# Kernel tuning notes

Measured on AMD Instinct MI355X. Metric: run time of the kernel, lower is better.

Reference implementation:

```python
import jax, jax.numpy as jnp
import numpy as np
import math

B, L, LC = 2, 2048, 2048
D_MODEL, D_CROSS, D_HEAD = 1024, 1024, 64
N_HEADS = D_MODEL // D_HEAD
D6 = D_HEAD // 6  # freq bands per spatial axis (k-diffusion AxialRoPE, 3 axes)
EPS = 1e-6


def rope_freqs():
    n = N_HEADS * D6
    f = jnp.exp(jnp.linspace(math.log(math.pi), math.log(10.0 * math.pi), n + 1)[:-1])
    return f.reshape(D6, N_HEADS).T  # [nh, d6]


def rope_theta(pos):
    # pos: [b, l, 3] -> theta: [b, nh, l, 3*d6]
    f = rope_freqs()
    th = jnp.concatenate([pos[..., None, a:a + 1] * f for a in range(3)], axis=-1)  # [b,l,nh,3*d6]
    return jnp.moveaxis(th, -2, -3)


def apply_rotary(x, theta):
    d = theta.shape[-1]
    x1, x2, x3 = x[..., :d], x[..., d:2 * d], x[..., 2 * d:]
    c, s = jnp.cos(theta), jnp.sin(theta)
    return jnp.concatenate([x1 * c - x2 * s, x2 * c + x1 * s, x3], axis=-1)


def rms_norm(x, scale, eps=EPS):
    ms = jnp.mean(x * x, axis=-1, keepdims=True)
    return x * (scale * jax.lax.rsqrt(ms + eps))


def cosine_scale(q, k, scale, eps=EPS):
    s = jnp.sqrt(scale)[:, None, None]  # [nh,1,1]
    qn = q * (s * jax.lax.rsqrt(jnp.sum(q * q, axis=-1, keepdims=True) + eps))
    kn = k * (s * jax.lax.rsqrt(jnp.sum(k * k, axis=-1, keepdims=True) + eps))
    return qn, kn


def setup_inputs():
    key = jax.random.key(0)
    ks = jax.random.split(key, 8)
    return {
        "x": jax.random.normal(ks[0], (B, L, D_MODEL), jnp.float32),
        "pos": jax.random.uniform(ks[1], (B, L, 3), jnp.float32),
        "x_cross": jax.random.normal(ks[2], (B, LC, D_CROSS), jnp.float32),
        "pos_cross": jax.random.uniform(ks[3], (B, LC, 3), jnp.float32),
        "norm_scale": jnp.ones((D_MODEL,), jnp.float32),
        "norm_cross_scale": jnp.ones((D_CROSS,), jnp.float32),
        "q_w": jax.random.normal(ks[4], (D_MODEL, D_MODEL), jnp.float32) * 0.02,
        "kv_w": jax.random.normal(ks[5], (2 * D_MODEL, D_CROSS), jnp.float32) * 0.02,
        "head_scale": jnp.full((N_HEADS,), 10.0, jnp.float32),
        "out_w": jax.random.normal(ks[6], (D_MODEL, D_MODEL), jnp.float32) * 0.02,
    }


def reference(x, pos, x_cross, pos_cross, norm_scale, norm_cross_scale, q_w, kv_w, head_scale, out_w):
    skip = x
    xn = rms_norm(x, norm_scale)
    xc = rms_norm(x_cross, norm_cross_scale)
    q = xn @ q_w.T                       # [b,l,d]
    kv = xc @ kv_w.T                     # [b,lc,2d]
    b, l, _ = q.shape
    lc = kv.shape[1]
    q = q.reshape(b, l, N_HEADS, D_HEAD).transpose(0, 2, 1, 3)          # [b,nh,l,e]
    kv = kv.reshape(b, lc, 2, N_HEADS, D_HEAD)                          # (t nh e) factorization
    k = kv[:, :, 0].transpose(0, 2, 1, 3)
    v = kv[:, :, 1].transpose(0, 2, 1, 3)
    q, k = cosine_scale(q, k, head_scale)
    q = apply_rotary(q, rope_theta(pos))
    k = apply_rotary(k, rope_theta(pos_cross))
    attn = jax.nn.softmax(jnp.einsum('bhqe,bhke->bhqk', q, k), axis=-1)  # scale=1.0 (cosine-sim pre-scaled)
    o = jnp.einsum('bhqk,bhke->bhqe', attn, v)
    o = o.transpose(0, 2, 1, 3).reshape(b, l, D_MODEL)
    return o @ out_w.T + skip
```

## Files before the change

kernel.cpp:

```cpp
#include <hip/hip_runtime.h>

typedef __bf16 bf16_t;
typedef __bf16 bf16x4 __attribute__((ext_vector_type(4)));
typedef __bf16 bf16x8 __attribute__((ext_vector_type(8)));
typedef float f32x4 __attribute__((ext_vector_type(4)));
typedef short s16x4 __attribute__((ext_vector_type(4)));

#define B_DIM 2
#define L_DIM 2048
#define LC_DIM 2048
#define DM 1024
#define NH 16
#define DH 64
#define MB (1u << 20)
#define LOG2E 1.44269504088896f
#define NZ 2
#define SPAN (LC_DIM / NZ)

__device__ __forceinline__ bool probe_is_f32(const unsigned* probe) {
  return probe[0] == 0x3F800000u;
}

__device__ __forceinline__ void async16(const bf16_t* g, bf16_t* l) {
  __builtin_amdgcn_global_load_lds((const __attribute__((address_space(1))) void*)g,
                                   (__attribute__((address_space(3))) void*)l, 16, 0, 0);
}

__device__ __forceinline__ f32x4 mfma16(bf16x4 a, bf16x4 b, f32x4 c) {
#if __has_builtin(__builtin_amdgcn_mfma_f32_16x16x16bf16_1k)
  union { bf16x4 h; s16x4 s; } ua, ub;
  ua.h = a; ub.h = b;
  return __builtin_amdgcn_mfma_f32_16x16x16bf16_1k(ua.s, ub.s, c, 0, 0, 0);
#else
  return c;
#endif
}

__device__ __forceinline__ void conv_b(const void* src, bf16_t* dst, int i, bool f32) {
  bf16x4 w;
  if (f32) {
    f32x4 v = *(const f32x4*)((const float*)src + i);
    w[0] = (bf16_t)v[0]; w[1] = (bf16_t)v[1]; w[2] = (bf16_t)v[2]; w[3] = (bf16_t)v[3];
  } else {
    w = *(const bf16x4*)((const bf16_t*)src + i);
  }
  *(bf16x4*)(dst + i) = w;
}
__device__ __forceinline__ void conv_f(const void* src, float* dst, int i, int n, bool f32) {
  if (i >= n) return;
  f32x4 v;
  if (f32) {
    v = *(const f32x4*)((const float*)src + i);
  } else {
    bf16x4 w = *(const bf16x4*)((const bf16_t*)src + i);
    v[0] = (float)w[0]; v[1] = (float)w[1]; v[2] = (float)w[2]; v[3] = (float)w[3];
  }
  *(f32x4*)(dst + i) = v;
}

__global__ __launch_bounds__(256) void front_k(
    const void* x, const void* xc, const void* qw, const void* kvw, const void* ow,
    const void* pos, const void* posc, const void* ns, const void* ncs, const void* hs,
    bf16_t* xn, bf16_t* xcn, bf16_t* cqw, bf16_t* ckvw, bf16_t* cow,
    float* fpos, float* fposc, float* fns, float* fncs, float* fhs,
    const unsigned* probe) {
  const bool f32 = probe_is_f32(probe);
  const int tid = threadIdx.x;
  if (blockIdx.x < 2 * B_DIM * L_DIM) {
    const bool isB = blockIdx.x >= B_DIM * L_DIM;
    const int row = isB ? blockIdx.x - B_DIM * L_DIM : blockIdx.x;
    const void* src = isB ? xc : x;
    const void* scr = isB ? ncs : ns;
    bf16_t* out = isB ? xcn : xn;
    float f0, f1, f2, f3, s0, s1, s2, s3;
    if (f32) {
      f32x4 v = *((const f32x4*)((const float*)src + (size_t)row * DM) + tid);
      f0 = v[0]; f1 = v[1]; f2 = v[2]; f3 = v[3];
      f32x4 sv = *((const f32x4*)scr + tid);
      s0 = sv[0]; s1 = sv[1]; s2 = sv[2]; s3 = sv[3];
    } else {
      bf16x4 v = *((const bf16x4*)((const bf16_t*)src + (size_t)row * DM) + tid);
      f0 = (float)v[0]; f1 = (float)v[1]; f2 = (float)v[2]; f3 = (float)v[3];
      bf16x4 sv = *((const bf16x4*)scr + tid);
      s0 = (float)sv[0]; s1 = (float)sv[1]; s2 = (float)sv[2]; s3 = (float)sv[3];
    }
    float ss = f0 * f0 + f1 * f1 + f2 * f2 + f3 * f3;
#pragma unroll
    for (int m = 1; m < 64; m <<= 1) ss += __shfl_xor(ss, m, 64);
    __shared__ float red[4];
    const int wave = tid >> 6, lane = tid & 63;
    if (lane == 0) red[wave] = ss;
    __syncthreads();
    float ms = (red[0] + red[1] + red[2] + red[3]) * (1.0f / DM);
    float r = rsqrtf(ms + 1e-6f);
    bf16x4 w;
    w[0] = (bf16_t)(f0 * r * s0);
    w[1] = (bf16_t)(f1 * r * s1);
    w[2] = (bf16_t)(f2 * r * s2);
    w[3] = (bf16_t)(f3 * r * s3);
    *(bf16x4*)(out + (size_t)row * DM + tid * 4) = w;
    return;
  }
  const int blk = blockIdx.x - 2 * B_DIM * L_DIM;
  const int e4 = tid * 4;
  if (blk < 1024)       conv_b(qw,  cqw,  blk * 1024 + e4, f32);
  else if (blk < 3072)  conv_b(kvw, ckvw, (blk - 1024) * 1024 + e4, f32);
  else if (blk < 4096)  conv_b(ow,  cow,  (blk - 3072) * 1024 + e4, f32);
  else if (blk < 4108)  conv_f(pos,  fpos,  (blk - 4096) * 1024 + e4, 12288, f32);
  else if (blk < 4120)  conv_f(posc, fposc, (blk - 4108) * 1024 + e4, 12288, f32);
  else if (blk == 4120) conv_f(ns,  fns,  e4, 1024, f32);
  else if (blk == 4121) conv_f(ncs, fncs, e4, 1024, f32);
  else                  conv_f(hs,  fhs,  e4, 16, f32);
}

__global__ __launch_bounds__(256) void gemm_qkv_k(const bf16_t* __restrict__ xn,
                                                  const bf16_t* __restrict__ xcn,
                                                  const bf16_t* __restrict__ qw,
                                                  const bf16_t* __restrict__ kvw,
                                                  bf16_t* __restrict__ qb,
                                                  bf16_t* __restrict__ kvK,
                                                  bf16_t* __restrict__ Vp) {
  __shared__ bf16_t Asm[128 * 32];
  __shared__ bf16_t Wsm[128 * 32];
  const int tid = threadIdx.x;
  const int wave = tid >> 6, lane = tid & 63;
  const int quad = lane >> 4, tc = lane & 15;
  const int wr = wave >> 1, wc = wave & 1;
  const bool isq = blockIdx.y < 8;
  const bf16_t* A = isq ? xn : xcn;
  const bf16_t* W = isq ? qw : kvw;
  const int n0 = (isq ? blockIdx.y : (blockIdx.y - 8)) * 128;
  const int m0 = blockIdx.x * 128;
  const int K = 1024;

  const int srow = wave * 16 + (lane >> 2);
  const int scol = (lane & 3) * 8;
  const bf16_t* ag = A + (size_t)(m0 + srow) * K + scol;
  const bf16_t* wg = W + (size_t)(n0 + srow) * K + scol;
  bf16_t* al0 = &Asm[(wave * 16) * 32];
  bf16_t* al1 = &Asm[(64 + wave * 16) * 32];
  bf16_t* wl0 = &Wsm[(wave * 16) * 32];
  bf16_t* wl1 = &Wsm[(64 + wave * 16) * 32];

  f32x4 acc[4][4] = {};

  for (int k0 = 0; k0 < K; k0 += 32) {
    async16(ag + k0, al0);
    async16(ag + k0 + (size_t)64 * K, al1);
    async16(wg + k0, wl0);
    async16(wg + k0 + (size_t)64 * K, wl1);
    __syncthreads();
    bf16x8 af[4], wf[4];
#pragma unroll
    for (int i = 0; i < 4; ++i)
      af[i] = *(const bf16x8*)&Asm[(wr * 64 + i * 16 + tc) * 32 + quad * 8];
#pragma unroll
    for (int j = 0; j < 4; ++j)
      wf[j] = *(const bf16x8*)&Wsm[(wc * 64 + j * 16 + tc) * 32 + quad * 8];
#pragma unroll
    for (int i = 0; i < 4; ++i)
#pragma unroll
      for (int j = 0; j < 4; ++j)
        acc[i][j] = __builtin_amdgcn_mfma_f32_16x16x32_bf16(af[i], wf[j], acc[i][j], 0, 0, 0);
    __syncthreads();
  }

  if (isq || n0 < DM) {
    bf16_t* C = isq ? qb : kvK;
#pragma unroll
    for (int i = 0; i < 4; ++i) {
      const size_t row = (size_t)m0 + wr * 64 + i * 16 + quad * 4;
#pragma unroll
      for (int j = 0; j < 4; ++j) {
        const int col = n0 + wc * 64 + j * 16 + tc;
#pragma unroll
        for (int r = 0; r < 4; ++r)
          C[(row + r) * DM + col] = (bf16_t)acc[i][j][r];
      }
    }
  } else {
#pragma unroll
    for (int i = 0; i < 4; ++i) {
      const int row = m0 + wr * 64 + i * 16 + quad * 4;
      const int b = row >> 11, kc = row & (LC_DIM - 1);
#pragma unroll
      for (int j = 0; j < 4; ++j) {
        const int hd = n0 - DM + wc * 64 + j * 16 + tc;
        const int h = hd >> 6, d = hd & 63;
        bf16x4 pk;
        pk[0] = (bf16_t)acc[i][j][0];
        pk[1] = (bf16_t)acc[i][j][1];
        pk[2] = (bf16_t)acc[i][j][2];
        pk[3] = (bf16_t)acc[i][j][3];
        *(bf16x4*)(Vp + (((size_t)(b * NH + h) * (LC_DIM / 4) + (kc >> 2)) * DH + d) * 4) = pk;
      }
    }
  }
}

__global__ __launch_bounds__(256) void prep_k(bf16_t* __restrict__ q,
                                              const bf16_t* __restrict__ kvK,
                                              bf16_t* __restrict__ Kp,
                                              const float* __restrict__ pos,
                                              const float* __restrict__ pos_cross,
                                              const float* __restrict__ head_scale) {
  const int gw = (blockIdx.x * blockDim.x + threadIdx.x) >> 6;
  const int lane = threadIdx.x & 63;
  const int per = B_DIM * L_DIM * NH;
  const bool is_k = gw >= per;
  const int id = is_k ? gw - per : gw;
  const int h = id & 15;
  const int row = id >> 4;
  const bf16_t* src = (is_k ? kvK : q) + (size_t)row * DM + h * DH;
  const float* pp = (is_k ? pos_cross : pos) + (size_t)row * 3;

  float val = (float)src[lane];
  float ss = val * val;
#pragma unroll
  for (int m = 1; m < 64; m <<= 1) ss += __shfl_xor(ss, m, 64);
  float sc = sqrtf(head_scale[h]) * rsqrtf(ss + 1e-6f);
  if (!is_k) sc *= LOG2E;
  float vn = val * sc;

  const int j = lane;
  const int tj = j < 30 ? j : (j < 60 ? j - 30 : 0);
  const int a = tj >= 20 ? 2 : (tj >= 10 ? 1 : 0);
  const int jj = tj - a * 10;
  float p = pp[a];
  float freq = 3.14159265358979f *
               __builtin_amdgcn_exp2f((float)(jj * 16 + h) * 0.0207620505930f);
  float rev = p * freq * 0.15915494309189535f;
  rev -= floorf(rev);
  float cth = __builtin_amdgcn_cosf(rev);
  float sth = __builtin_amdgcn_sinf(rev);
  const int partner = j < 30 ? j + 30 : (j < 60 ? j - 30 : j);
  float vp = __shfl(vn, partner, 64);
  float outv;
  if (j < 30)       outv = vn * cth - vp * sth;
  else if (j < 60)  outv = vn * cth + vp * sth;
  else              outv = vn;

  if (is_k) {
    const int b = row >> 11, l = row & (LC_DIM - 1);
    const int dsw = (((lane >> 3) ^ (l & 7)) << 3) | (lane & 7);
    Kp[(((size_t)b * NH + h) * LC_DIM + l) * DH + dsw] = (bf16_t)outv;
  } else {
    q[(size_t)row * DM + h * DH + lane] = (bf16_t)outv;
  }
}

#define STAGE14(BUF, KC)                                                         \
  {                                                                              \
    const bf16_t* ks_ = kg + (size_t)(KC) * DH;                                  \
    const bf16_t* vs_ = vg + (size_t)((KC) >> 2) * (DH * 4);                     \
    const int so_ = wave * 1024 + lane * 8;                                      \
    async16(ks_ + so_, &Kl[BUF][wave * 1024]);                                   \
    async16(ks_ + so_ + 512, &Kl[BUF][wave * 1024 + 512]);                       \
    async16(vs_ + so_, &Vl[BUF][wave * 1024]);                                   \
    async16(vs_ + so_ + 512, &Vl[BUF][wave * 1024 + 512]);                       \
  }

#define COMPUTE14(BUF)                                                           \
  {                                                                              \
    bf16x8 KB[4][2];                                                             \
    _Pragma("unroll") for (int mt = 0; mt < 4; ++mt)                             \
      _Pragma("unroll") for (int hf = 0; hf < 2; ++hf)                           \
        KB[mt][hf] = *(const bf16x8*)&Kl[BUF][(mt * 16 + tc) * 64 +              \
                                              (((hf << 2) | quad) ^ (tc & 7)) * 8]; \
    bf16x4 p[2][4];                                                              \
    _Pragma("unroll") for (int qg = 0; qg < 2; ++qg) {                           \
      f32x4 s[4];                                                                \
      _Pragma("unroll") for (int mt = 0; mt < 4; ++mt) {                         \
        f32x4 zf = {0.f, 0.f, 0.f, 0.f};                                         \
        zf = __builtin_amdgcn_mfma_f32_16x16x32_bf16(KB[mt][0], qf[qg][0], zf, 0, 0, 0); \
        zf = __builtin_amdgcn_mfma_f32_16x16x32_bf16(KB[mt][1], qf[qg][1], zf, 0, 0, 0); \
        s[mt] = zf;                                                              \
      }                                                                          \
      _Pragma("unroll") for (int mt = 0; mt < 4; ++mt) {                         \
        p[qg][mt][0] = (bf16_t)__builtin_amdgcn_exp2f(s[mt][0]);                 \
        p[qg][mt][1] = (bf16_t)__builtin_amdgcn_exp2f(s[mt][1]);                 \
        p[qg][mt][2] = (bf16_t)__builtin_amdgcn_exp2f(s[mt][2]);                 \
        p[qg][mt][3] = (bf16_t)__builtin_amdgcn_exp2f(s[mt][3]);                 \
      }                                                                          \
    }                                                                            \
    bf16x4 VB[4][4];                                                             \
    _Pragma("unroll") for (int mt = 0; mt < 4; ++mt)                             \
      _Pragma("unroll") for (int dt = 0; dt < 4; ++dt)                           \
        VB[mt][dt] = *(const bf16x4*)&Vl[BUF][(mt * 4 + quad) * 256 +            \
                                              (dt * 16 + tc) * 4];               \
    _Pragma("unroll") for (int qg = 0; qg < 2; ++qg)                             \
      _Pragma("unroll") for (int mt = 0; mt < 4; ++mt) {                         \
        accL[qg] = mfma16(p[qg][mt], ones, accL[qg]);                            \
        _Pragma("unroll") for (int dt = 0; dt < 4; ++dt)                         \
          accO[qg][dt] = mfma16(p[qg][mt], VB[mt][dt], accO[qg][dt]);            \
      }                                                                          \
  }

__global__ __launch_bounds__(256, 3) void flash14_k(const bf16_t* __restrict__ q,
                                                    const bf16_t* __restrict__ Kp,
                                                    const bf16_t* __restrict__ Vp,
                                                    bf16_t* __restrict__ Op,
                                                    float* __restrict__ lp) {
  const int tid = threadIdx.x;
  const int wave = tid >> 6, lane = tid & 63;
  const int quad = lane >> 4, tc = lane & 15;
  const int bh = blockIdx.y, b = bh >> 4;
  const int z = blockIdx.z;
  const int qr = blockIdx.x * 128 + wave * 32;

  __shared__ bf16_t Kl[2][64 * 64];
  __shared__ bf16_t Vl[2][64 * 64];

  bf16x8 qf[2][2];
#pragma unroll
  for (int qg = 0; qg < 2; ++qg)
#pragma unroll
    for (int hf = 0; hf < 2; ++hf)
      qf[qg][hf] = *(const bf16x8*)(q + (size_t)(b * L_DIM + qr + qg * 16 + tc) * DM +
                                    (bh & 15) * DH + hf * 32 + quad * 8);

  f32x4 accO[2][4] = {};
  f32x4 accL[2] = {};
  bf16x4 ones;
  ones[0] = (bf16_t)1.0f; ones[1] = (bf16_t)1.0f;
  ones[2] = (bf16_t)1.0f; ones[3] = (bf16_t)1.0f;

  const bf16_t* kg = Kp + (size_t)bh * LC_DIM * DH;
  const bf16_t* vg = Vp + (size_t)bh * (LC_DIM / 4) * DH * 4;
  const int base = z * SPAN;

  STAGE14(0, base);
  __syncthreads();
  int cur = 0;
#pragma unroll 1
  for (int t = 0; t < SPAN / 64; ++t) {
    if (t + 1 < SPAN / 64) STAGE14(cur ^ 1, base + (t + 1) * 64);
    COMPUTE14(cur);
    __syncthreads();
    cur ^= 1;
  }

  bf16_t* Ob = Op + (size_t)(z * 32 + bh) * L_DIM * DH;
  float* lb = lp + (size_t)(z * 32 + bh) * L_DIM;
#pragma unroll
  for (int qg = 0; qg < 2; ++qg) {
    if (tc == 0) {
#pragma unroll
      for (int r = 0; r < 4; ++r) lb[qr + qg * 16 + quad * 4 + r] = accL[qg][r];
    }
#pragma unroll
    for (int r = 0; r < 4; ++r) {
      const size_t qg_row = (size_t)qr + qg * 16 + quad * 4 + r;
#pragma unroll
      for (int dt = 0; dt < 4; ++dt)
        Ob[qg_row * DH + dt * 16 + tc] = (bf16_t)accO[qg][dt][r];
    }
  }
}

__global__ __launch_bounds__(256) void gemm_out_k(const bf16_t* __restrict__ Op,
                                                  const float* __restrict__ lp,
                                                  const bf16_t* __restrict__ W,
                                                  const void* __restrict__ skip_raw,
                                                  void* __restrict__ out,
                                                  const unsigned* __restrict__ probe) {
  __shared__ bf16_t Asm[64 * 32];
  __shared__ bf16_t Wsm[128 * 32];
  const int tid = threadIdx.x;
  const int wave = tid >> 6, lane = tid & 63;
  const int quad = lane >> 4, tc = lane & 15;
  const int wr = wave >> 1, wc = wave & 1;
  const int m0 = blockIdx.x * 64, n0 = blockIdx.y * 128;
  const int K = 1024, N = 1024;

  const int srow = wave * 16 + (lane >> 2);
  const int scol = (lane & 3) * 8;
  const int arow = m0 + srow;
  const int bb = arow >> 11, l = arow & (L_DIM - 1);
  const size_t zoff = (size_t)32 * L_DIM * DH;
  const bf16_t* wg = W + (size_t)(n0 + srow) * K + scol;
  bf16_t* wl0 = &Wsm[(wave * 16) * 32];
  bf16_t* wl1 = &Wsm[(64 + wave * 16) * 32];

  f32x4 acc[2][4] = {};

  float lv0 = lp[(size_t)(bb * NH) * L_DIM + l];
  float lv1 = lp[(size_t)(32 + bb * NH) * L_DIM + l];
  bf16x8 a0 = *(const bf16x8*)(Op + ((size_t)(bb * NH) * L_DIM + l) * DH + scol);
  bf16x8 a1 = *(const bf16x8*)(Op + zoff + ((size_t)(bb * NH) * L_DIM + l) * DH + scol);

  for (int k0 = 0; k0 < K; k0 += 32) {
    async16(wg + k0, wl0);
    async16(wg + k0 + (size_t)64 * K, wl1);
    const float linv = 1.f / (lv0 + lv1);
    bf16x8 aw;
#pragma unroll
    for (int e = 0; e < 8; ++e)
      aw[e] = (bf16_t)(((float)a0[e] + (float)a1[e]) * linv);
    *(bf16x8*)&Asm[srow * 32 + scol] = aw;
    if (k0 + 32 < K) {
      const int kn = k0 + 32;
      const int bhn = bb * NH + (kn >> 6);
      if ((kn & 63) == 0) {
        lv0 = lp[(size_t)bhn * L_DIM + l];
        lv1 = lp[(size_t)(32 + bhn) * L_DIM + l];
      }
      const size_t obn = ((size_t)bhn * L_DIM + l) * DH + (kn & 63) + scol;
      a0 = *(const bf16x8*)(Op + obn);
      a1 = *(const bf16x8*)(Op + zoff + obn);
    }
    __syncthreads();
    bf16x8 af[2], wf[4];
#pragma unroll
    for (int i = 0; i < 2; ++i)
      af[i] = *(const bf16x8*)&Asm[(wr * 32 + i * 16 + tc) * 32 + quad * 8];
#pragma unroll
    for (int j = 0; j < 4; ++j)
      wf[j] = *(const bf16x8*)&Wsm[(wc * 64 + j * 16 + tc) * 32 + quad * 8];
#pragma unroll
    for (int i = 0; i < 2; ++i)
#pragma unroll
      for (int j = 0; j < 4; ++j)
        acc[i][j] = __builtin_amdgcn_mfma_f32_16x16x32_bf16(af[i], wf[j], acc[i][j], 0, 0, 0);
    __syncthreads();
  }

  const bool f32o = probe_is_f32(probe);
#pragma unroll
  for (int i = 0; i < 2; ++i) {
    const size_t row = (size_t)m0 + wr * 32 + i * 16 + quad * 4;
#pragma unroll
    for (int j = 0; j < 4; ++j) {
      const int col = n0 + wc * 64 + j * 16 + tc;
#pragma unroll
      for (int r = 0; r < 4; ++r) {
        const size_t idx = (row + r) * (size_t)N + col;
        float v = acc[i][j][r];
        if (f32o) {
          v += ((const float*)skip_raw)[idx];
          ((float*)out)[idx] = v;
        } else {
          v += (float)((const bf16_t*)skip_raw)[idx];
          ((bf16_t*)out)[idx] = (bf16_t)v;
        }
      }
    }
  }
}

extern "C" void kernel_launch(void* const* d_in, const int* in_sizes, int n_in,
                              void* d_out, int out_size, void* d_ws, size_t ws_size,
                              hipStream_t stream) {
  const unsigned* probe = (const unsigned*)d_in[4];
  char* ws = (char*)d_ws;

  bf16_t* cow  = (bf16_t*)(ws + 0 * MB);
  bf16_t* cqw  = (bf16_t*)(ws + 2 * MB);
  bf16_t* ckvw = (bf16_t*)(ws + 4 * MB);
  bf16_t* xn   = (bf16_t*)(ws + 8 * MB);
  bf16_t* xcn  = (bf16_t*)(ws + 16 * MB);
  bf16_t* Op   = (bf16_t*)(ws + 8 * MB);
  bf16_t* kvK  = (bf16_t*)(ws + 24 * MB);
  bf16_t* qb   = (bf16_t*)(ws + 32 * MB);
  bf16_t* Vp   = (bf16_t*)(ws + 40 * MB);
  bf16_t* Kp   = (bf16_t*)(ws + 48 * MB);
  float* lp    = (float*)(ws + 64 * MB);
  float* fpos  = (float*)(ws + 65 * MB);
  float* fposc = (float*)(ws + 65 * MB + 64 * 1024);
  float* fns   = (float*)(ws + 65 * MB + 128 * 1024);
  float* fncs  = (float*)(ws + 65 * MB + 144 * 1024);
  float* fhs   = (float*)(ws + 65 * MB + 160 * 1024);

  front_k<<<2 * B_DIM * L_DIM + 4123, 256, 0, stream>>>(
      d_in[0], d_in[2], d_in[6], d_in[7], d_in[9], d_in[1], d_in[3], d_in[4],
      d_in[5], d_in[8], xn, xcn, cqw, ckvw, cow, fpos, fposc, fns, fncs, fhs, probe);
  gemm_qkv_k<<<dim3(32, 24), 256, 0, stream>>>(xn, xcn, cqw, ckvw, qb, kvK, Vp);
  prep_k<<<(2 * B_DIM * L_DIM * NH) / 4, 256, 0, stream>>>(qb, kvK, Kp, fpos, fposc, fhs);
  flash14_k<<<dim3(L_DIM / 128, B_DIM * NH, NZ), 256, 0, stream>>>(qb, Kp, Vp, Op, lp);
  gemm_out_k<<<dim3(64, 8), 256, 0, stream>>>(Op, lp, cow, d_in[0], d_out, probe);
}
```

Before: 254.8 us.

## Double-buffer LDS tiles in QKV and output GEMMs to overlap loads with MFMA

Both projection GEMMs now keep two LDS tile buffers and issue the next k-slice's async global-to-LDS loads before running MFMAs on the current slice. This cuts the loop from two barriers per step to one and is meant to hide global load latency behind compute. It doubles LDS use per block, which may lower occupancy. Correctness depends on the async LDS writes being complete at the single barrier, since there is no explicit vmcnt wait.

```diff
diff --git a/kernel.cpp b/kernel.cpp
--- a/kernel.cpp
+++ b/kernel.cpp
@@ -113,6 +113,14 @@
   else                  conv_f(hs,  fhs,  e4, 16, f32);
 }
 
+#define QKV_STAGE(BUF, KO)                                                       \
+  {                                                                              \
+    async16(ag + (KO), &Asm[BUF][(wave * 16) * 32]);                             \
+    async16(ag + (KO) + (size_t)64 * K, &Asm[BUF][(64 + wave * 16) * 32]);       \
+    async16(wg + (KO), &Wsm[BUF][(wave * 16) * 32]);                             \
+    async16(wg + (KO) + (size_t)64 * K, &Wsm[BUF][(64 + wave * 16) * 32]);       \
+  }
+
 __global__ __launch_bounds__(256) void gemm_qkv_k(const bf16_t* __restrict__ xn,
                                                   const bf16_t* __restrict__ xcn,
                                                   const bf16_t* __restrict__ qw,
@@ -120,8 +128,8 @@
                                                   bf16_t* __restrict__ qb,
                                                   bf16_t* __restrict__ kvK,
                                                   bf16_t* __restrict__ Vp) {
-  __shared__ bf16_t Asm[128 * 32];
-  __shared__ bf16_t Wsm[128 * 32];
+  __shared__ bf16_t Asm[2][128 * 32];
+  __shared__ bf16_t Wsm[2][128 * 32];
   const int tid = threadIdx.x;
   const int wave = tid >> 6, lane = tid & 63;
   const int quad = lane >> 4, tc = lane & 15;
@@ -137,32 +145,28 @@
   const int scol = (lane & 3) * 8;
   const bf16_t* ag = A + (size_t)(m0 + srow) * K + scol;
   const bf16_t* wg = W + (size_t)(n0 + srow) * K + scol;
-  bf16_t* al0 = &Asm[(wave * 16) * 32];
-  bf16_t* al1 = &Asm[(64 + wave * 16) * 32];
-  bf16_t* wl0 = &Wsm[(wave * 16) * 32];
-  bf16_t* wl1 = &Wsm[(64 + wave * 16) * 32];
 
   f32x4 acc[4][4] = {};
 
+  QKV_STAGE(0, 0);
+  __syncthreads();
+  int cur = 0;
   for (int k0 = 0; k0 < K; k0 += 32) {
-    async16(ag + k0, al0);
-    async16(ag + k0 + (size_t)64 * K, al1);
-    async16(wg + k0, wl0);
-    async16(wg + k0 + (size_t)64 * K, wl1);
-    __syncthreads();
+    if (k0 + 32 < K) QKV_STAGE(cur ^ 1, k0 + 32);
     bf16x8 af[4], wf[4];
 #pragma unroll
     for (int i = 0; i < 4; ++i)
-      af[i] = *(const bf16x8*)&Asm[(wr * 64 + i * 16 + tc) * 32 + quad * 8];
+      af[i] = *(const bf16x8*)&Asm[cur][(wr * 64 + i * 16 + tc) * 32 + quad * 8];
 #pragma unroll
     for (int j = 0; j < 4; ++j)
-      wf[j] = *(const bf16x8*)&Wsm[(wc * 64 + j * 16 + tc) * 32 + quad * 8];
+      wf[j] = *(const bf16x8*)&Wsm[cur][(wc * 64 + j * 16 + tc) * 32 + quad * 8];
 #pragma unroll
     for (int i = 0; i < 4; ++i)
 #pragma unroll
       for (int j = 0; j < 4; ++j)
         acc[i][j] = __builtin_amdgcn_mfma_f32_16x16x32_bf16(af[i], wf[j], acc[i][j], 0, 0, 0);
     __syncthreads();
+    cur ^= 1;
   }
 
   if (isq || n0 < DM) {
@@ -358,14 +362,20 @@
   }
 }
 
+#define OUT_STAGE_W(BUF, KO)                                                     \
+  {                                                                              \
+    async16(wg + (KO), &Wsm[BUF][(wave * 16) * 32]);                             \
+    async16(wg + (KO) + (size_t)64 * K, &Wsm[BUF][(64 + wave * 16) * 32]);       \
+  }
+
 __global__ __launch_bounds__(256) void gemm_out_k(const bf16_t* __restrict__ Op,
                                                   const float* __restrict__ lp,
                                                   const bf16_t* __restrict__ W,
                                                   const void* __restrict__ skip_raw,
                                                   void* __restrict__ out,
                                                   const unsigned* __restrict__ probe) {
-  __shared__ bf16_t Asm[64 * 32];
-  __shared__ bf16_t Wsm[128 * 32];
+  __shared__ bf16_t Asm[2][64 * 32];
+  __shared__ bf16_t Wsm[2][128 * 32];
   const int tid = threadIdx.x;
   const int wave = tid >> 6, lane = tid & 63;
   const int quad = lane >> 4, tc = lane & 15;
@@ -379,8 +389,6 @@
   const int bb = arow >> 11, l = arow & (L_DIM - 1);
   const size_t zoff = (size_t)32 * L_DIM * DH;
   const bf16_t* wg = W + (size_t)(n0 + srow) * K + scol;
-  bf16_t* wl0 = &Wsm[(wave * 16) * 32];
-  bf16_t* wl1 = &Wsm[(64 + wave * 16) * 32];
 
   f32x4 acc[2][4] = {};
 
@@ -389,40 +397,59 @@
   bf16x8 a0 = *(const bf16x8*)(Op + ((size_t)(bb * NH) * L_DIM + l) * DH + scol);
   bf16x8 a1 = *(const bf16x8*)(Op + zoff + ((size_t)(bb * NH) * L_DIM + l) * DH + scol);
 
-  for (int k0 = 0; k0 < K; k0 += 32) {
-    async16(wg + k0, wl0);
-    async16(wg + k0 + (size_t)64 * K, wl1);
+  OUT_STAGE_W(0, 0);
+  {
     const float linv = 1.f / (lv0 + lv1);
     bf16x8 aw;
 #pragma unroll
     for (int e = 0; e < 8; ++e)
       aw[e] = (bf16_t)(((float)a0[e] + (float)a1[e]) * linv);
-    *(bf16x8*)&Asm[srow * 32 + scol] = aw;
-    if (k0 + 32 < K) {
-      const int kn = k0 + 32;
-      const int bhn = bb * NH + (kn >> 6);
-      if ((kn & 63) == 0) {
-        lv0 = lp[(size_t)bhn * L_DIM + l];
-        lv1 = lp[(size_t)(32 + bhn) * L_DIM + l];
+    *(bf16x8*)&Asm[0][srow * 32 + scol] = aw;
+  }
+  {
+    const size_t obn = ((size_t)(bb * NH) * L_DIM + l) * DH + 32 + scol;
+    a0 = *(const bf16x8*)(Op + obn);
+    a1 = *(const bf16x8*)(Op + zoff + obn);
+  }
+  __syncthreads();
+
+  int cur = 0;
+  for (int k0 = 0; k0 < K; k0 += 32) {
+    const bool has_next = k0 + 32 < K;
+    if (has_next) {
+      OUT_STAGE_W(cur ^ 1, k0 + 32);
+      const float linv = 1.f / (lv0 + lv1);
+      bf16x8 aw;
+#pragma unroll
+      for (int e = 0; e < 8; ++e)
+        aw[e] = (bf16_t)(((float)a0[e] + (float)a1[e]) * linv);
+      *(bf16x8*)&Asm[cur ^ 1][srow * 32 + scol] = aw;
+      if (k0 + 64 < K) {
+        const int kn = k0 + 64;
+        const int bhn = bb * NH + (kn >> 6);
+        if ((kn & 63) == 0) {
+          lv0 = lp[(size_t)bhn * L_DIM + l];
+          lv1 = lp[(size_t)(32 + bhn) * L_DIM + l];
+        }
+        const size_t obn = ((size_t)bhn * L_DIM + l) * DH + (kn & 63) + scol;
+        a0 = *(const bf16x8*)(Op + obn);
+        a1 = *(const bf16x8*)(Op + zoff + obn);
       }
-      const size_t obn = ((size_t)bhn * L_DIM + l) * DH + (kn & 63) + scol;
-      a0 = *(const bf16x8*)(Op + obn);
-      a1 = *(const bf16x8*)(Op + zoff + obn);
-    }
-    __syncthreads();
+    }
     bf16x8 af[2], wf[4];
 #pragma unroll
     for (int i = 0; i < 2; ++i)
-      af[i] = *(const bf16x8*)&Asm[(wr * 32 + i * 16 + tc) * 32 + quad * 8];
+      af[i] = *(const bf16x8*)&Asm[cur][(wr * 32 + i * 16 + tc) * 32 + quad * 8];
 #pragma unroll
     for (int j = 0; j < 4; ++j)
-      wf[j] = *(const bf16x8*)&Wsm[(wc * 64 + j * 16 + tc) * 32 + quad * 8];
+      wf[j] = *(const bf16x8*)&Wsm[cur][(wc * 64 + j * 16 + tc) * 32 + quad * 8];
 #pragma unroll
     for (int i = 0; i < 2; ++i)
 #pragma unroll
       for (int j = 0; j < 4; ++j)
         acc[i][j] = __builtin_amdgcn_mfma_f32_16x16x32_bf16(af[i], wf[j], acc[i][j], 0, 0, 0);
     __syncthreads();
+    cur ^= 1;
   }
 
   const bool f32o = probe_is_f32(probe);
```

After: 240.0 us. 5.8% less time.
